# Kernel optimization log

Hardware: AMD Instinct MI355X
Metric: run time of the kernel (lower is better)

Reference implementation:

```python
import jax, jax.numpy as jnp
import numpy as np

# snntorch Leaky defaults / CFG constants
BETA = 0.9      # CFG.lif_beta
IAPP = 0.0      # CFG.Iapp
THR = 1.0       # snn.Leaky default threshold
SLOPE = 25.0    # surrogate.fast_sigmoid default slope


@jax.custom_vjp
def spike(x):
    # Heaviside spike with fast-sigmoid surrogate gradient
    return (x > 0).astype(x.dtype)

def _spike_fwd(x):
    return spike(x), x

def _spike_bwd(x, g):
    return (g / (SLOPE * jnp.abs(x) + 1.0) ** 2,)

spike.defvjp(_spike_fwd, _spike_bwd)


def setup_inputs() -> dict:
    key = jax.random.key(0)
    z = jax.random.normal(key, (32, 1024, 512), dtype=jnp.float32)
    return {"z": z}


def reference(z):
    # z: [B, T, H]; sequential LIF over time axis.
    # snntorch Leaky (reset='subtract'):
    #   reset = detach(V_prev > thr)
    #   V_k   = beta * V_prev + input_k - reset * thr
    #   spk_k = heaviside(V_k - thr)
    # Original loop: input at step k is z[:, k-1] + Iapp (noise std = 0.0).
    B, T, H = z.shape
    zt = jnp.transpose(z[:, :-1, :], (1, 0, 2))  # [T-1, B, H]
    V0 = jnp.zeros((B, H), dtype=z.dtype)

    def step(V, zin):
        reset = jax.lax.stop_gradient((V > THR).astype(V.dtype))
        Vn = BETA * V + (zin + IAPP) - reset * THR
        spk = spike(Vn - THR)
        return Vn, spk

    _, spks = jax.lax.scan(step, V0, zt)  # spks: [T-1, B, H]
    # T[:, 0, :] stays zero (loop starts at k=1)
    Tout = jnp.concatenate(
        [jnp.zeros((B, 1, H), dtype=z.dtype), jnp.transpose(spks, (1, 0, 2))],
        axis=1,
    )
    return Tout
```

## Files before the change

### kernel.cpp

```cpp
#include <hip/hip_runtime.h>


#define LIF_H 512
#define TS 32

__global__ __launch_bounds__(64, 1) void lif_kernel(const float* __restrict__ z,
                                                    float* __restrict__ out) {
    __shared__ float Abuf[TS * 64];
    __shared__ float Bbuf[TS * 64];

    const int t = threadIdx.x;
    const int blk = blockIdx.x;
    const int b = blk >> 3;
    const int h0 = (blk & 7) << 6;
    const size_t base = (size_t)b * (1024 * LIF_H) + h0 + t;

    const float* zp = z + base;
    float* op = out + base;

    op[0] = 0.0f;

    float r[TS];

#pragma unroll
    for (int j = 0; j < TS; ++j) r[j] = zp[(size_t)j * LIF_H];
#pragma unroll
    for (int j = 0; j < TS; ++j) Abuf[j * 64 + t] = r[j];

    float V = 0.0f;

    for (int k = 0; k < 31; ++k) {
        const float* cur = (k & 1) ? Bbuf : Abuf;
        float* nxt = (k & 1) ? Abuf : Bbuf;

#pragma unroll
        for (int j = 0; j < TS; ++j)
            r[j] = zp[(size_t)((k + 1) * TS + j) * LIF_H];

#pragma unroll
        for (int i = 0; i < TS; ++i) {
            const float zv = cur[i * 64 + t];
            const float v0 = __fadd_rn(__fmul_rn(0.9f, V), zv);
            const float Vn = (V > 1.0f) ? __fsub_rn(v0, 1.0f) : v0;
            op[(size_t)(k * TS + i + 1) * LIF_H] = (Vn > 1.0f) ? 1.0f : 0.0f;
            V = Vn;
        }

#pragma unroll
        for (int j = 0; j < TS; ++j) nxt[j * 64 + t] = r[j];
    }

#pragma unroll
    for (int i = 0; i < TS - 1; ++i) {
        const float zv = Bbuf[i * 64 + t];
        const float v0 = __fadd_rn(__fmul_rn(0.9f, V), zv);
        const float Vn = (V > 1.0f) ? __fsub_rn(v0, 1.0f) : v0;
        op[(size_t)(31 * TS + i + 1) * LIF_H] = (Vn > 1.0f) ? 1.0f : 0.0f;
        V = Vn;
    }
}

extern "C" void kernel_launch(void* const* d_in, const int* in_sizes, int n_in,
                              void* d_out, int out_size, void* d_ws, size_t ws_size,
                              hipStream_t stream) {
    const float* z = (const float*)d_in[0];
    float* out = (float*)d_out;
    dim3 block(64);
    dim3 grid(256);
    hipLaunchKernelGGL(lif_kernel, grid, block, 0, stream, z, out);
}
```

Before: 132.8 us.

## Replace LDS double buffer with triple-buffered register prefetch pipeline

Drops the shared-memory staging of input tiles and instead keeps three 32-float register buffers rotated so that two tiles of global loads are in flight while one is computed. Empty asm statements force the loaded values to be materialized at chosen points, so the compiler cannot sink the loads next to their uses. This removes the LDS write/read traffic and raises prefetch depth, at the cost of more VGPRs per thread, which is fine with only one 64-thread block per CU.

```diff
diff --git a/kernel.cpp b/kernel.cpp
--- a/kernel.cpp
+++ b/kernel.cpp
@@ -4,11 +4,39 @@
 #define LIF_H 512
 #define TS 32
 
+__device__ __forceinline__ void load32(float (&r)[TS], const float* zp, int tile) {
+    const float* s = zp + (size_t)tile * TS * LIF_H;
+#pragma unroll
+    for (int j = 0; j < TS; ++j) r[j] = s[(size_t)j * LIF_H];
+}
+
+__device__ __forceinline__ void launder32(float (&r)[TS]) {
+    asm volatile("" : "+v"(r[0]), "+v"(r[1]), "+v"(r[2]), "+v"(r[3]),
+                      "+v"(r[4]), "+v"(r[5]), "+v"(r[6]), "+v"(r[7]),
+                      "+v"(r[8]), "+v"(r[9]), "+v"(r[10]), "+v"(r[11]),
+                      "+v"(r[12]), "+v"(r[13]), "+v"(r[14]), "+v"(r[15]));
+    asm volatile("" : "+v"(r[16]), "+v"(r[17]), "+v"(r[18]), "+v"(r[19]),
+                      "+v"(r[20]), "+v"(r[21]), "+v"(r[22]), "+v"(r[23]),
+                      "+v"(r[24]), "+v"(r[25]), "+v"(r[26]), "+v"(r[27]),
+                      "+v"(r[28]), "+v"(r[29]), "+v"(r[30]), "+v"(r[31]));
+}
+
+template <int SN>
+__device__ __forceinline__ float compute_tile(const float (&r)[TS], int tile,
+                                              float V, float* __restrict__ op) {
+    float* o = op + (size_t)(tile * TS + 1) * LIF_H;
+#pragma unroll
+    for (int i = 0; i < SN; ++i) {
+        const float v0 = __fadd_rn(__fmul_rn(0.9f, V), r[i]);
+        const float Vn = (V > 1.0f) ? __fsub_rn(v0, 1.0f) : v0;
+        o[(size_t)i * LIF_H] = (Vn > 1.0f) ? 1.0f : 0.0f;
+        V = Vn;
+    }
+    return V;
+}
+
 __global__ __launch_bounds__(64, 1) void lif_kernel(const float* __restrict__ z,
                                                     float* __restrict__ out) {
-    __shared__ float Abuf[TS * 64];
-    __shared__ float Bbuf[TS * 64];
-
     const int t = threadIdx.x;
     const int blk = blockIdx.x;
     const int b = blk >> 3;
@@ -20,44 +48,31 @@
 
     op[0] = 0.0f;
 
-    float r[TS];
+    float rA[TS], rB[TS], rC[TS];
 
-#pragma unroll
-    for (int j = 0; j < TS; ++j) r[j] = zp[(size_t)j * LIF_H];
-#pragma unroll
-    for (int j = 0; j < TS; ++j) Abuf[j * 64 + t] = r[j];
+    load32(rA, zp, 0);
+    load32(rB, zp, 1);
+    launder32(rA);
 
     float V = 0.0f;
 
-    for (int k = 0; k < 31; ++k) {
-        const float* cur = (k & 1) ? Bbuf : Abuf;
-        float* nxt = (k & 1) ? Abuf : Bbuf;
+    for (int m = 0; m < 30; m += 3) {
+        load32(rC, zp, m + 2);
+        V = compute_tile<TS>(rA, m, V, op);
+        launder32(rB);
 
-#pragma unroll
-        for (int j = 0; j < TS; ++j)
-            r[j] = zp[(size_t)((k + 1) * TS + j) * LIF_H];
+        load32(rA, zp, m + 3);
+        V = compute_tile<TS>(rB, m + 1, V, op);
+        launder32(rC);
 
-#pragma unroll
-        for (int i = 0; i < TS; ++i) {
-            const float zv = cur[i * 64 + t];
-            const float v0 = __fadd_rn(__fmul_rn(0.9f, V), zv);
-            const float Vn = (V > 1.0f) ? __fsub_rn(v0, 1.0f) : v0;
-            op[(size_t)(k * TS + i + 1) * LIF_H] = (Vn > 1.0f) ? 1.0f : 0.0f;
-            V = Vn;
-        }
-
-#pragma unroll
-        for (int j = 0; j < TS; ++j) nxt[j * 64 + t] = r[j];
+        load32(rB, zp, m + 4);
+        V = compute_tile<TS>(rC, m + 2, V, op);
+        launder32(rA);
     }
 
-#pragma unroll
-    for (int i = 0; i < TS - 1; ++i) {
-        const float zv = Bbuf[i * 64 + t];
-        const float v0 = __fadd_rn(__fmul_rn(0.9f, V), zv);
-        const float Vn = (V > 1.0f) ? __fsub_rn(v0, 1.0f) : v0;
-        op[(size_t)(31 * TS + i + 1) * LIF_H] = (Vn > 1.0f) ? 1.0f : 0.0f;
-        V = Vn;
-    }
+    V = compute_tile<TS>(rA, 30, V, op);
+    launder32(rB);
+    compute_tile<TS - 1>(rB, 31, V, op);
 }
 
 extern "C" void kernel_launch(void* const* d_in, const int* in_sizes, int n_in,
```

Result: faster. 120.8 us (-9.1%).
